# Performance work log

Hardware: AMD Instinct MI355X
Metric: run time of the kernel (lower is better)

Reference implementation:

```python
import jax, jax.numpy as jnp
import numpy as np

DIM = 256
N_EMBED = 8192
BETA = 0.25


def setup_inputs() -> dict:
    key = jax.random.key(0)
    k1, k2, k3, k4 = jax.random.split(key, 4)
    inp = {
        "input": jax.random.normal(k1, (16, 1024, DIM), dtype=jnp.float32),
        # nn.Embedding weight init: normal(0, dim**-0.5)
        "embed_weight": jax.random.normal(k2, (N_EMBED, DIM), dtype=jnp.float32) * (DIM ** -0.5),
        # nn.Linear(dim, dim): weight [out, in], bias [out]
        "proj_w": jax.random.normal(k3, (DIM, DIM), dtype=jnp.float32) * (DIM ** -0.5),
        "proj_b": jax.random.normal(k4, (DIM,), dtype=jnp.float32) * 0.01,
    }
    return inp


def reference(input, embed_weight, proj_w, proj_b):
    flatten = input.reshape(-1, DIM)                      # [N, d]
    # projected codebook: Linear(embedding.weight)
    quant_codebook = embed_weight @ proj_w.T + proj_b     # [K, d]
    d = (jnp.sum(flatten ** 2, axis=1, keepdims=True)
         + jnp.sum(quant_codebook ** 2, axis=1)
         - 2.0 * jnp.einsum('nd,kd->nk', flatten, quant_codebook))  # [N, K]
    min_encoding_indices = jnp.argmin(d, axis=1)          # [N]
    z_quantize = quant_codebook[min_encoding_indices].reshape(input.shape)
    sg = jax.lax.stop_gradient
    diff = jnp.mean((sg(z_quantize) - input) ** 2)
    commit_loss = jnp.mean((z_quantize - sg(input)) ** 2)
    diff = diff + BETA * commit_loss                      # legacy=True branch
    # straight-through estimator
    z_quantize = input + sg(z_quantize - input)
    return (z_quantize, diff, min_encoding_indices)
```

## Files before the change

### kernel.cpp

```cpp
#include <hip/hip_runtime.h>

#define DIMD   256
#define NTOK   16384
#define NCODE  8192
#define NELEM  (NTOK * DIMD)

#define BM 128
#define BK 128
#define BD 32
#define PAD 4
#define LDS_STRIDE (BM + PAD)

#define SPLITS_B 4
#define CODES_PER_WAVE (NCODE / SPLITS_B / 4)
#define NGROUPS (CODES_PER_WAVE / 16)
#define MARGIN 0.5f
#define EBUF_CAP 1024

typedef float floatx4 __attribute__((ext_vector_type(4)));
typedef short short8  __attribute__((ext_vector_type(8)));

__device__ __forceinline__ unsigned short f2bf(float f) {
    unsigned u = __float_as_uint(f);
    unsigned r = (u + 0x7FFFu + ((u >> 16) & 1u)) >> 16;
    return (unsigned short)r;
}

__device__ __forceinline__ unsigned fkey(float f) {
    unsigned u = __float_as_uint(f);
    return (u & 0x80000000u) ? ~u : (u | 0x80000000u);
}
__device__ __forceinline__ float funkey(unsigned k) {
    unsigned u = (k & 0x80000000u) ? (k & 0x7FFFFFFFu) : ~k;
    return __uint_as_float(u);
}

__device__ __forceinline__ size_t cb2_idx(int row, int col) {
    return ((size_t)((row >> 4) * 8 + (col >> 5))) * 512
         + (size_t)((((col >> 3) & 3) * 16 + (row & 15)) * 8 + (col & 7));
}

__global__ __launch_bounds__(256, 3)
void project_kernel(const float* __restrict__ E, const float* __restrict__ W,
                    const float* __restrict__ bias, float* __restrict__ C,
                    unsigned short* __restrict__ Cb2, float* __restrict__ cnorm)
{
    __shared__ float smem[2 * BD * LDS_STRIDE];
    float* As = smem;
    float* Bs = smem + BD * LDS_STRIDE;

    const int tid = threadIdx.x;
    const int tx  = tid & 15;
    const int ty  = tid >> 4;
    const int m0  = blockIdx.x * BM;
    const int j0  = blockIdx.y * BK;

    const int srow = tid >> 3;
    const int scol = (tid & 7) * 4;

    float acc[8][8];
#pragma unroll
    for (int i = 0; i < 8; ++i)
#pragma unroll
        for (int j = 0; j < 8; ++j) acc[i][j] = 0.f;

    for (int dc = 0; dc < DIMD / BD; ++dc) {
        const int d0 = dc * BD;
        __syncthreads();
#pragma unroll
        for (int rr = 0; rr < 4; ++rr) {
            const int r = srow + rr * 32;
            float4 av = *(const float4*)&E[(size_t)(m0 + r) * DIMD + d0 + scol];
            As[(scol + 0) * LDS_STRIDE + r] = av.x;
            As[(scol + 1) * LDS_STRIDE + r] = av.y;
            As[(scol + 2) * LDS_STRIDE + r] = av.z;
            As[(scol + 3) * LDS_STRIDE + r] = av.w;
            float4 bv = *(const float4*)&W[(size_t)(j0 + r) * DIMD + d0 + scol];
            Bs[(scol + 0) * LDS_STRIDE + r] = bv.x;
            Bs[(scol + 1) * LDS_STRIDE + r] = bv.y;
            Bs[(scol + 2) * LDS_STRIDE + r] = bv.z;
            Bs[(scol + 3) * LDS_STRIDE + r] = bv.w;
        }
        __syncthreads();
#pragma unroll 4
        for (int d = 0; d < BD; ++d) {
            float4 a0 = *(float4*)&As[d * LDS_STRIDE + ty * 4];
            float4 a1 = *(float4*)&As[d * LDS_STRIDE + 64 + ty * 4];
            float4 b0 = *(float4*)&Bs[d * LDS_STRIDE + tx * 4];
            float4 b1 = *(float4*)&Bs[d * LDS_STRIDE + 64 + tx * 4];
            float a[8] = {a0.x, a0.y, a0.z, a0.w, a1.x, a1.y, a1.z, a1.w};
            float b[8] = {b0.x, b0.y, b0.z, b0.w, b1.x, b1.y, b1.z, b1.w};
#pragma unroll
            for (int i = 0; i < 8; ++i)
#pragma unroll
                for (int j = 0; j < 8; ++j) acc[i][j] = fmaf(a[i], b[j], acc[i][j]);
        }
    }

    __syncthreads();
    float* red = smem;

    float4 bja = *(const float4*)&bias[j0 + tx * 4];
    float4 bjb = *(const float4*)&bias[j0 + 64 + tx * 4];
#pragma unroll
    for (int i = 0; i < 8; ++i) {
        const int mloc = (i < 4) ? (ty * 4 + i) : (64 + ty * 4 + (i - 4));
        const int row  = m0 + mloc;
        const size_t rbase = (size_t)row * DIMD;
        float o[8] = {acc[i][0] + bja.x, acc[i][1] + bja.y, acc[i][2] + bja.z, acc[i][3] + bja.w,
                      acc[i][4] + bjb.x, acc[i][5] + bjb.y, acc[i][6] + bjb.z, acc[i][7] + bjb.w};
        *(float4*)&C[rbase + j0 + tx * 4]      = *(float4*)&o[0];
        *(float4*)&C[rbase + j0 + 64 + tx * 4] = *(float4*)&o[4];
        ushort4 h0 = {f2bf(o[0]), f2bf(o[1]), f2bf(o[2]), f2bf(o[3])};
        ushort4 h1 = {f2bf(o[4]), f2bf(o[5]), f2bf(o[6]), f2bf(o[7])};
        *(ushort4*)&Cb2[cb2_idx(row, j0 + tx * 4)]      = h0;
        *(ushort4*)&Cb2[cb2_idx(row, j0 + 64 + tx * 4)] = h1;
        float p = 0.f;
#pragma unroll
        for (int j = 0; j < 8; ++j) p = fmaf(o[j], o[j], p);
        red[mloc * 16 + tx] = p;
    }
    __syncthreads();
    if (tid < 128) {
        float s = 0.f;
#pragma unroll
        for (int k = 0; k < 16; ++k) s += red[tid * 16 + k];
        atomicAdd(&cnorm[m0 + tid], s);
    }
}

__global__ void convx_kernel(const float* __restrict__ X, float* __restrict__ xnorm,
                             unsigned short* __restrict__ Xb)
{
    const int wave = threadIdx.x >> 6;
    const int lane = threadIdx.x & 63;
    const int row  = blockIdx.x * 4 + wave;
    float4 v = *(const float4*)&X[(size_t)row * DIMD + lane * 4];
    ushort4 h = {f2bf(v.x), f2bf(v.y), f2bf(v.z), f2bf(v.w)};
    *(ushort4*)&Xb[(size_t)row * DIMD + lane * 4] = h;
    float s = v.x * v.x + v.y * v.y + v.z * v.z + v.w * v.w;
#pragma unroll
    for (int off = 1; off < 64; off <<= 1) s += __shfl_xor(s, off);
    if (lane == 0) xnorm[row] = s;
}

__global__ __launch_bounds__(256, 2)
void dist_min_kernel(const unsigned short* __restrict__ Xb,
                     const unsigned short* __restrict__ Cb2,
                     const float* __restrict__ cnorm,
                     unsigned* __restrict__ minkey)
{
    __shared__ float wmin[4][32];

    const int tid  = threadIdx.x;
    const int lane = tid & 63;
    const int wv   = tid >> 6;
    const int l15  = lane & 15;
    const int quad = lane >> 4;
    const int tok0 = blockIdx.x * 32;
    const int cbase = blockIdx.y * (NCODE / SPLITS_B) + wv * CODES_PER_WAVE;

    short8 a[2][8];
#pragma unroll
    for (int i = 0; i < 2; ++i) {
        const unsigned short* ap = Xb + (size_t)(tok0 + i * 16 + l15) * DIMD + quad * 8;
#pragma unroll
        for (int ks = 0; ks < 8; ++ks)
            a[i][ks] = *(const short8*)(ap + ks * 32);
    }

    float runv[8];
#pragma unroll
    for (int s = 0; s < 8; ++s) runv[s] = 3.4e38f;

    const unsigned short* bp0 = Cb2 + (size_t)cbase * DIMD + lane * 8;

    short8 breg[2][8];
    float  cnr[2];
#pragma unroll
    for (int ks = 0; ks < 8; ++ks) breg[0][ks] = *(const short8*)(bp0 + ks * 512);
    cnr[0] = cnorm[cbase + l15];

    auto group_body = [&](int g, short8 (&bc)[8], short8 (&bn)[8],
                          float cnc, float& cnn) {
        if (g + 1 < NGROUPS) {
            const unsigned short* bpn = bp0 + (size_t)(g + 1) * 4096;
#pragma unroll
            for (int ks = 0; ks < 8; ++ks) bn[ks] = *(const short8*)(bpn + ks * 512);
            cnn = cnorm[cbase + (g + 1) * 16 + l15];
        }

        floatx4 acc[2];
#pragma unroll
        for (int i = 0; i < 2; ++i) acc[i] = (floatx4){0.f, 0.f, 0.f, 0.f};
#pragma unroll
        for (int ks = 0; ks < 8; ++ks)
#pragma unroll
            for (int i = 0; i < 2; ++i)
                acc[i] = __builtin_amdgcn_mfma_f32_16x16x32_bf16(a[i][ks], bc[ks], acc[i], 0, 0, 0);

#pragma unroll
        for (int i = 0; i < 2; ++i)
#pragma unroll
            for (int r = 0; r < 4; ++r)
                runv[i * 4 + r] = fminf(runv[i * 4 + r], fmaf(-2.f, acc[i][r], cnc));
    };

    for (int gg = 0; gg < NGROUPS; gg += 2) {
        group_body(gg,     breg[0], breg[1], cnr[0], cnr[1]);
        group_body(gg + 1, breg[1], breg[0], cnr[1], cnr[0]);
    }

#pragma unroll
    for (int s = 0; s < 8; ++s) {
        float m = runv[s];
#pragma unroll
        for (int off = 1; off < 16; off <<= 1) m = fminf(m, __shfl_xor(m, off));
        runv[s] = m;
    }
    if (l15 == 0) {
#pragma unroll
        for (int i = 0; i < 2; ++i)
#pragma unroll
            for (int r = 0; r < 4; ++r)
                wmin[wv][i * 16 + quad * 4 + r] = runv[i * 4 + r];
    }
    __syncthreads();
    if (tid < 32) {
        const float bm = fminf(fminf(wmin[0][tid], wmin[1][tid]),
                               fminf(wmin[2][tid], wmin[3][tid]));
        atomicMin(&minkey[tok0 + tid], fkey(bm));
    }
}

__global__ __launch_bounds__(256, 2)
void dist_emit_kernel(const unsigned short* __restrict__ Xb,
                      const unsigned short* __restrict__ Cb2,
                      const float* __restrict__ cnorm,
                      const unsigned* __restrict__ minkey,
                      unsigned* __restrict__ list, unsigned* __restrict__ count,
                      unsigned cap)
{
    __shared__ float tokthr[64];
    __shared__ unsigned ebuf[EBUF_CAP];
    __shared__ unsigned ecnt, gbase;

    const int tid  = threadIdx.x;
    const int lane = tid & 63;
    const int wv   = tid >> 6;
    const int l15  = lane & 15;
    const int quad = lane >> 4;
    const int tok0 = blockIdx.x * 64;
    const int cbase = blockIdx.y * (NCODE / SPLITS_B) + wv * CODES_PER_WAVE;

    if (tid == 0) ecnt = 0;
    if (tid < 64) tokthr[tid] = funkey(minkey[tok0 + tid]) + MARGIN;
    __syncthreads();

    short8 a[4][8];
#pragma unroll
    for (int i = 0; i < 4; ++i) {
        const unsigned short* ap = Xb + (size_t)(tok0 + i * 16 + l15) * DIMD + quad * 8;
#pragma unroll
        for (int ks = 0; ks < 8; ++ks)
            a[i][ks] = *(const short8*)(ap + ks * 32);
    }

    float thr[16];
#pragma unroll
    for (int i = 0; i < 4; ++i)
#pragma unroll
        for (int r = 0; r < 4; ++r)
            thr[i * 4 + r] = tokthr[i * 16 + quad * 4 + r];

    const unsigned short* bp0 = Cb2 + (size_t)cbase * DIMD + lane * 8;

    short8 breg[2][8];
    float  cnr[2];
#pragma unroll
    for (int ks = 0; ks < 8; ++ks) breg[0][ks] = *(const short8*)(bp0 + ks * 512);
    cnr[0] = cnorm[cbase + l15];

    auto group_body = [&](int g, short8 (&bc)[8], short8 (&bn)[8],
                          float cnc, float& cnn) {
        const int code0 = cbase + g * 16;
        if (g + 1 < NGROUPS) {
            const unsigned short* bpn = bp0 + (size_t)(g + 1) * 4096;
#pragma unroll
            for (int ks = 0; ks < 8; ++ks) bn[ks] = *(const short8*)(bpn + ks * 512);
            cnn = cnorm[code0 + 16 + l15];
        }

        floatx4 acc[4];
#pragma unroll
        for (int i = 0; i < 4; ++i) acc[i] = (floatx4){0.f, 0.f, 0.f, 0.f};
#pragma unroll
        for (int ks = 0; ks < 8; ++ks)
#pragma unroll
            for (int i = 0; i < 4; ++i)
                acc[i] = __builtin_amdgcn_mfma_f32_16x16x32_bf16(a[i][ks], bc[ks], acc[i], 0, 0, 0);

        unsigned mask = 0;
#pragma unroll
        for (int i = 0; i < 4; ++i)
#pragma unroll
            for (int r = 0; r < 4; ++r) {
                const float dd = fmaf(-2.f, acc[i][r], cnc);
                if (dd < thr[i * 4 + r]) mask |= (1u << (i * 4 + r));
            }

        if (__any(mask != 0)) {
            if (mask) {
                unsigned pos = atomicAdd(&ecnt, (unsigned)__popc(mask));
#pragma unroll
                for (int i = 0; i < 4; ++i)
#pragma unroll
                    for (int r = 0; r < 4; ++r) {
                        const int s = i * 4 + r;
                        if (mask & (1u << s)) {
                            const unsigned token = tok0 + i * 16 + quad * 4 + r;
                            const unsigned entry = (token << 13) | (unsigned)(code0 + l15);
                            if (pos < EBUF_CAP) ebuf[pos] = entry;
                            else { unsigned gp = atomicAdd(count, 1u); if (gp < cap) list[gp] = entry; }
                            ++pos;
                        }
                    }
            }
        }
    };

    for (int gg = 0; gg < NGROUPS; gg += 2) {
        group_body(gg,     breg[0], breg[1], cnr[0], cnr[1]);
        group_body(gg + 1, breg[1], breg[0], cnr[1], cnr[0]);
    }

    __syncthreads();
    const unsigned n = (ecnt < EBUF_CAP) ? ecnt : EBUF_CAP;
    if (tid == 0) gbase = atomicAdd(count, n);
    __syncthreads();
    const unsigned gb = gbase;
    for (unsigned i = tid; i < n; i += 256) {
        const unsigned p = gb + i;
        if (p < cap) list[p] = ebuf[i];
    }
}

__global__ __launch_bounds__(256)
void rescore_kernel(const float* __restrict__ X, const float* __restrict__ C,
                    const float* __restrict__ xnorm, const float* __restrict__ cnorm,
                    const unsigned* __restrict__ list, const unsigned* __restrict__ count,
                    unsigned cap, unsigned long long* __restrict__ fin)
{
    const int lane = threadIdx.x & 63;
    const int g16  = lane & 15;
    const int sub  = lane >> 4;
    const int gid  = ((blockIdx.x * 256 + threadIdx.x) >> 6) * 4 + sub;
    const int ng   = ((gridDim.x * 256) >> 6) * 4;
    unsigned n = *count; if (n > cap) n = cap;

    for (unsigned c = gid; c < n; c += ng) {
        const unsigned e = list[c];
        const unsigned tok = e >> 13, code = e & 8191u;
        const float* xr = &X[(size_t)tok * DIMD];
        const float* cr = &C[(size_t)code * DIMD];
        float dot = 0.f;
#pragma unroll
        for (int r = 0; r < 4; ++r) {
            float4 x4 = *(const float4*)&xr[r * 64 + g16 * 4];
            float4 c4 = *(const float4*)&cr[r * 64 + g16 * 4];
            dot = fmaf(x4.x, c4.x, dot);
            dot = fmaf(x4.y, c4.y, dot);
            dot = fmaf(x4.z, c4.z, dot);
            dot = fmaf(x4.w, c4.w, dot);
        }
#pragma unroll
        for (int d = 1; d < 16; d <<= 1) dot += __shfl_xor(dot, d);
        if (g16 == 0) {
            const float dd = xnorm[tok] + cnorm[code] - 2.f * dot;
            const unsigned long long p =
                ((unsigned long long)__float_as_uint(dd) << 32) | code;
            atomicMin(&fin[tok], p);
        }
    }
}

__global__ __launch_bounds__(256)
void finalize_kernel(const float* __restrict__ X, const float* __restrict__ C,
                     const unsigned long long* __restrict__ fin,
                     float* __restrict__ out)
{
    __shared__ float part[4];
    const int lane = threadIdx.x & 63;
    const int wv   = threadIdx.x >> 6;
    const int t0   = blockIdx.x * 64;

    float local = 0.f;
    for (int it = 0; it < 16; ++it) {
        const int t = t0 + wv * 16 + it;
        const unsigned code = (unsigned)(fin[t] & 0xFFFFFFFFull);
        float4 c4 = *(const float4*)&C[(size_t)code * DIMD + lane * 4];
        float4 x4 = *(const float4*)&X[(size_t)t * DIMD + lane * 4];
        float4 w  = {c4.x - x4.x, c4.y - x4.y, c4.z - x4.z, c4.w - x4.w};
        local += w.x * w.x + w.y * w.y + w.z * w.z + w.w * w.w;
        float4 zq = {x4.x + w.x, x4.y + w.y, x4.z + w.z, x4.w + w.w};
        *(float4*)&out[(size_t)t * DIMD + lane * 4] = zq;
        if (lane == 0) out[NELEM + 1 + t] = (float)code;
    }
#pragma unroll
    for (int off = 1; off < 64; off <<= 1) local += __shfl_xor(local, off);
    if (lane == 0) part[wv] = local;
    __syncthreads();
    if (threadIdx.x == 0) {
        const float s = part[0] + part[1] + part[2] + part[3];
        atomicAdd(&out[NELEM], s * (1.25f / (float)NELEM));
    }
}

extern "C" void kernel_launch(void* const* d_in, const int* in_sizes, int n_in,
                              void* d_out, int out_size, void* d_ws, size_t ws_size,
                              hipStream_t stream)
{
    const float* X = (const float*)d_in[0];
    const float* E = (const float*)d_in[1];
    const float* W = (const float*)d_in[2];
    const float* b = (const float*)d_in[3];
    float* out = (float*)d_out;

    char* w = (char*)d_ws;
    float* C            = (float*)w;           w += (size_t)NCODE * DIMD * 4;
    unsigned short* Xb  = (unsigned short*)w;  w += (size_t)NTOK * DIMD * 2;
    unsigned short* Cb2 = (unsigned short*)w;  w += (size_t)NCODE * DIMD * 2;
    float* xnorm        = (float*)w;           w += (size_t)NTOK * 4;
    float* cnorm        = (float*)w;           w += (size_t)NCODE * 4;
    unsigned* cnt       = (unsigned*)w;        w += 256;
    unsigned long long* fin = (unsigned long long*)w; w += (size_t)NTOK * 8;
    unsigned* minkey    = (unsigned*)w;        w += (size_t)NTOK * 4;
    unsigned* list      = (unsigned*)w;

    size_t used = (size_t)(w - (char*)d_ws);
    size_t avail = (ws_size > used) ? (ws_size - used) / 4 : 0;
    unsigned cap = (unsigned)((avail > 16777216u) ? 16777216u : avail);

    hipMemsetAsync(cnorm, 0, (size_t)NCODE * 4 + 256, stream);
    hipMemsetAsync(fin, 0xFF, (size_t)NTOK * 8 + (size_t)NTOK * 4, stream);
    hipMemsetAsync(out + NELEM, 0, 4, stream);

    project_kernel<<<dim3(NCODE / BM, DIMD / BK), 256, 0, stream>>>(E, W, b, C, Cb2, cnorm);
    convx_kernel<<<NTOK / 4, 256, 0, stream>>>(X, xnorm, Xb);
    dist_min_kernel<<<dim3(NTOK / 32, SPLITS_B), 256, 0, stream>>>(
        Xb, Cb2, cnorm, minkey);
    dist_emit_kernel<<<dim3(NTOK / 64, SPLITS_B), 256, 0, stream>>>(
        Xb, Cb2, cnorm, minkey, list, cnt, cap);
    rescore_kernel<<<1024, 256, 0, stream>>>(X, C, xnorm, cnorm, list, cnt, cap, fin);
    finalize_kernel<<<NTOK / 64, 256, 0, stream>>>(X, C, fin, out);
}
```

Baseline: 306.3 us.

## Stage codebook tiles via direct global-to-LDS loads and widen min-kernel token tile

Both distance kernels now stream each wave's codebook group into a double-buffered LDS region using global_load_lds with a two-deep prefetch, and preload codebook norms into LDS. This replaces the register double-buffering of B fragments and is meant to free VGPRs and hide global latency. The min kernel also doubles its token tile from 32 to 64 per block, so each B fragment is reused across four MFMA rows instead of two and codebook traffic is halved. The change adds 64KB+ of LDS per block, which may lower occupancy, and relies on hand-written waitcnt ordering being correct.

```diff
diff --git a/kernel.cpp b/kernel.cpp
--- a/kernel.cpp
+++ b/kernel.cpp
@@ -19,11 +19,18 @@
 
 typedef float floatx4 __attribute__((ext_vector_type(4)));
 typedef short short8  __attribute__((ext_vector_type(8)));
+typedef unsigned int u32;
 
 __device__ __forceinline__ unsigned short f2bf(float f) {
     unsigned u = __float_as_uint(f);
     unsigned r = (u + 0x7FFFu + ((u >> 16) & 1u)) >> 16;
     return (unsigned short)r;
+}
+
+__device__ __forceinline__ void gl_lds16(const void* g, void* l) {
+    __builtin_amdgcn_global_load_lds(
+        (const __attribute__((address_space(1))) u32*)g,
+        (__attribute__((address_space(3))) u32*)l, 16, 0, 0);
 }
 
 __device__ __forceinline__ unsigned fkey(float f) {
@@ -150,69 +157,74 @@
                      const float* __restrict__ cnorm,
                      unsigned* __restrict__ minkey)
 {
-    __shared__ float wmin[4][32];
+    __shared__ short Bls[4][2][4096];
+    __shared__ float cnl[4][CODES_PER_WAVE];
+    __shared__ float wmin[4][64];
 
     const int tid  = threadIdx.x;
     const int lane = tid & 63;
     const int wv   = tid >> 6;
     const int l15  = lane & 15;
     const int quad = lane >> 4;
-    const int tok0 = blockIdx.x * 32;
+    const int tok0 = blockIdx.x * 64;
     const int cbase = blockIdx.y * (NCODE / SPLITS_B) + wv * CODES_PER_WAVE;
 
-    short8 a[2][8];
-#pragma unroll
-    for (int i = 0; i < 2; ++i) {
+    gl_lds16(cnorm + cbase + 0   + lane * 4, &cnl[wv][0]);
+    gl_lds16(cnorm + cbase + 256 + lane * 4, &cnl[wv][256]);
+
+    const unsigned short* bsrc = Cb2 + (size_t)cbase * DIMD;
+    auto STAGE = [&](int g) {
+        const unsigned short* s = bsrc + (size_t)g * 4096 + lane * 8;
+        short* d = &Bls[wv][g & 1][0];
+#pragma unroll
+        for (int j = 0; j < 8; ++j)
+            gl_lds16(s + j * 512, d + j * 512);
+    };
+    STAGE(0);
+    STAGE(1);
+
+    short8 a[4][8];
+#pragma unroll
+    for (int i = 0; i < 4; ++i) {
         const unsigned short* ap = Xb + (size_t)(tok0 + i * 16 + l15) * DIMD + quad * 8;
 #pragma unroll
         for (int ks = 0; ks < 8; ++ks)
             a[i][ks] = *(const short8*)(ap + ks * 32);
     }
 
-    float runv[8];
-#pragma unroll
-    for (int s = 0; s < 8; ++s) runv[s] = 3.4e38f;
-
-    const unsigned short* bp0 = Cb2 + (size_t)cbase * DIMD + lane * 8;
-
-    short8 breg[2][8];
-    float  cnr[2];
-#pragma unroll
-    for (int ks = 0; ks < 8; ++ks) breg[0][ks] = *(const short8*)(bp0 + ks * 512);
-    cnr[0] = cnorm[cbase + l15];
-
-    auto group_body = [&](int g, short8 (&bc)[8], short8 (&bn)[8],
-                          float cnc, float& cnn) {
-        if (g + 1 < NGROUPS) {
-            const unsigned short* bpn = bp0 + (size_t)(g + 1) * 4096;
-#pragma unroll
-            for (int ks = 0; ks < 8; ++ks) bn[ks] = *(const short8*)(bpn + ks * 512);
-            cnn = cnorm[cbase + (g + 1) * 16 + l15];
-        }
-
-        floatx4 acc[2];
-#pragma unroll
-        for (int i = 0; i < 2; ++i) acc[i] = (floatx4){0.f, 0.f, 0.f, 0.f};
+    float runv[16];
+#pragma unroll
+    for (int s = 0; s < 16; ++s) runv[s] = 3.4e38f;
+
+    for (int g = 0; g < NGROUPS; ++g) {
+        asm volatile("s_waitcnt vmcnt(8)" ::: "memory");
+        const short* bp = &Bls[wv][g & 1][lane * 8];
+        short8 bc[8];
+#pragma unroll
+        for (int ks = 0; ks < 8; ++ks) bc[ks] = *(const short8*)(bp + ks * 512);
+        const float cnc = cnl[wv][g * 16 + l15];
+        asm volatile("s_waitcnt lgkmcnt(0)" ::: "memory");
+        __builtin_amdgcn_sched_barrier(0);
+        if (g + 2 < NGROUPS) STAGE(g + 2);
+
+        floatx4 acc[4];
+#pragma unroll
+        for (int i = 0; i < 4; ++i) acc[i] = (floatx4){0.f, 0.f, 0.f, 0.f};
 #pragma unroll
         for (int ks = 0; ks < 8; ++ks)
 #pragma unroll
-            for (int i = 0; i < 2; ++i)
+            for (int i = 0; i < 4; ++i)
                 acc[i] = __builtin_amdgcn_mfma_f32_16x16x32_bf16(a[i][ks], bc[ks], acc[i], 0, 0, 0);
 
 #pragma unroll
-        for (int i = 0; i < 2; ++i)
+        for (int i = 0; i < 4; ++i)
 #pragma unroll
             for (int r = 0; r < 4; ++r)
                 runv[i * 4 + r] = fminf(runv[i * 4 + r], fmaf(-2.f, acc[i][r], cnc));
-    };
-
-    for (int gg = 0; gg < NGROUPS; gg += 2) {
-        group_body(gg,     breg[0], breg[1], cnr[0], cnr[1]);
-        group_body(gg + 1, breg[1], breg[0], cnr[1], cnr[0]);
-    }
-
-#pragma unroll
-    for (int s = 0; s < 8; ++s) {
+    }
+
+#pragma unroll
+    for (int s = 0; s < 16; ++s) {
         float m = runv[s];
 #pragma unroll
         for (int off = 1; off < 16; off <<= 1) m = fminf(m, __shfl_xor(m, off));
@@ -220,13 +232,13 @@
     }
     if (l15 == 0) {
 #pragma unroll
-        for (int i = 0; i < 2; ++i)
+        for (int i = 0; i < 4; ++i)
 #pragma unroll
             for (int r = 0; r < 4; ++r)
                 wmin[wv][i * 16 + quad * 4 + r] = runv[i * 4 + r];
     }
     __syncthreads();
-    if (tid < 32) {
+    if (tid < 64) {
         const float bm = fminf(fminf(wmin[0][tid], wmin[1][tid]),
                                fminf(wmin[2][tid], wmin[3][tid]));
         atomicMin(&minkey[tok0 + tid], fkey(bm));
@@ -241,6 +253,8 @@
                       unsigned* __restrict__ list, unsigned* __restrict__ count,
                       unsigned cap)
 {
+    __shared__ short Bls[4][2][4096];
+    __shared__ float cnl[4][CODES_PER_WAVE];
     __shared__ float tokthr[64];
     __shared__ unsigned ebuf[EBUF_CAP];
     __shared__ unsigned ecnt, gbase;
@@ -253,6 +267,20 @@
     const int tok0 = blockIdx.x * 64;
     const int cbase = blockIdx.y * (NCODE / SPLITS_B) + wv * CODES_PER_WAVE;
 
+    gl_lds16(cnorm + cbase + 0   + lane * 4, &cnl[wv][0]);
+    gl_lds16(cnorm + cbase + 256 + lane * 4, &cnl[wv][256]);
+
+    const unsigned short* bsrc = Cb2 + (size_t)cbase * DIMD;
+    auto STAGE = [&](int g) {
+        const unsigned short* s = bsrc + (size_t)g * 4096 + lane * 8;
+        short* d = &Bls[wv][g & 1][0];
+#pragma unroll
+        for (int j = 0; j < 8; ++j)
+            gl_lds16(s + j * 512, d + j * 512);
+    };
+    STAGE(0);
+    STAGE(1);
+
     if (tid == 0) ecnt = 0;
     if (tid < 64) tokthr[tid] = funkey(minkey[tok0 + tid]) + MARGIN;
     __syncthreads();
@@ -273,23 +301,17 @@
         for (int r = 0; r < 4; ++r)
             thr[i * 4 + r] = tokthr[i * 16 + quad * 4 + r];
 
-    const unsigned short* bp0 = Cb2 + (size_t)cbase * DIMD + lane * 8;
-
-    short8 breg[2][8];
-    float  cnr[2];
-#pragma unroll
-    for (int ks = 0; ks < 8; ++ks) breg[0][ks] = *(const short8*)(bp0 + ks * 512);
-    cnr[0] = cnorm[cbase + l15];
-
-    auto group_body = [&](int g, short8 (&bc)[8], short8 (&bn)[8],
-                          float cnc, float& cnn) {
+    for (int g = 0; g < NGROUPS; ++g) {
         const int code0 = cbase + g * 16;
-        if (g + 1 < NGROUPS) {
-            const unsigned short* bpn = bp0 + (size_t)(g + 1) * 4096;
-#pragma unroll
-            for (int ks = 0; ks < 8; ++ks) bn[ks] = *(const short8*)(bpn + ks * 512);
-            cnn = cnorm[code0 + 16 + l15];
-        }
+        asm volatile("s_waitcnt vmcnt(8)" ::: "memory");
+        const short* bp = &Bls[wv][g & 1][lane * 8];
+        short8 bc[8];
+#pragma unroll
+        for (int ks = 0; ks < 8; ++ks) bc[ks] = *(const short8*)(bp + ks * 512);
+        const float cnc = cnl[wv][g * 16 + l15];
+        asm volatile("s_waitcnt lgkmcnt(0)" ::: "memory");
+        __builtin_amdgcn_sched_barrier(0);
+        if (g + 2 < NGROUPS) STAGE(g + 2);
 
         floatx4 acc[4];
 #pragma unroll
@@ -327,11 +349,6 @@
                     }
             }
         }
-    };
-
-    for (int gg = 0; gg < NGROUPS; gg += 2) {
-        group_body(gg,     breg[0], breg[1], cnr[0], cnr[1]);
-        group_body(gg + 1, breg[1], breg[0], cnr[1], cnr[0]);
     }
 
     __syncthreads();
@@ -447,7 +464,7 @@
 
     project_kernel<<<dim3(NCODE / BM, DIMD / BK), 256, 0, stream>>>(E, W, b, C, Cb2, cnorm);
     convx_kernel<<<NTOK / 4, 256, 0, stream>>>(X, xnorm, Xb);
-    dist_min_kernel<<<dim3(NTOK / 32, SPLITS_B), 256, 0, stream>>>(
+    dist_min_kernel<<<dim3(NTOK / 64, SPLITS_B), 256, 0, stream>>>(
         Xb, Cb2, cnorm, minkey);
     dist_emit_kernel<<<dim3(NTOK / 64, SPLITS_B), 256, 0, stream>>>(
         Xb, Cb2, cnorm, minkey, list, cnt, cap);
```

New measurement: 305.2 us. Within noise of the previous version (-0.4%).
